# Performance work log

Measured on AMD Instinct MI355X. Metric: run time of the kernel, lower is better.

The kernel has to match this reference:

```python
import jax, jax.numpy as jnp
import numpy as np

B, D1, DJ, S, OUT = 8, 1024, 512, 2048, 2048
IN = D1 + 2 * DJ  # linear input_dim = 2048


def setup_inputs() -> dict:
    key = jax.random.key(0)
    k1, k2, k3, kw, kb = jax.random.split(key, 5)
    return {
        "input1": jax.random.normal(k1, (B, D1, S), dtype=jnp.float32),
        "input2_a": jax.random.normal(k2, (B, DJ, S), dtype=jnp.float32),
        "input2_b": jax.random.normal(k3, (B, DJ, S), dtype=jnp.float32),
        "W": jax.random.normal(kw, (OUT, IN), dtype=jnp.float32) * (1.0 / np.sqrt(IN)),
        "b": jax.random.normal(kb, (OUT,), dtype=jnp.float32) * 0.01,
    }


def reference(input1, input2_a, input2_b, W, b):
    # Original loops over seq_len, per-step concat along feature dim then linear.
    # Fused: concat along feature axis once, transpose to [B, S, F], one GEMM.
    x = jnp.concatenate([input1, input2_a, input2_b], axis=1)  # [B, IN, S]
    x = jnp.transpose(x, (0, 2, 1))                            # [B, S, IN]
    out = jnp.einsum('bsf,of->bso', x, W) + b                  # [B, S, OUT]
    return out
```

## Files before the change

### kernel.cpp

```cpp
#include <hip/hip_runtime.h>
#include <hip/hip_bf16.h>

#define B_   8
#define D1_  1024
#define DJ_  512
#define S_   2048
#define OUT_ 2048
#define IN_  2048
#define M_TOT (B_ * S_)

typedef __attribute__((ext_vector_type(8))) short          bf16x8;
typedef __attribute__((ext_vector_type(8))) unsigned short ushort8;
typedef __attribute__((ext_vector_type(4))) float          f32x4;

typedef __attribute__((address_space(3))) unsigned int as3_uint;
typedef __attribute__((address_space(1))) unsigned int as1_uint;

__device__ __forceinline__ unsigned short f2bf(float f) {
    union { float f; unsigned u; } v; v.f = f;
    unsigned r = v.u + 0x7FFF + ((v.u >> 16) & 1);
    return (unsigned short)(r >> 16);
}

__device__ __forceinline__ void gload_lds16(const void* g, const void* l) {
    __builtin_amdgcn_global_load_lds(
        (const as1_uint*)(unsigned long long)g,
        (as3_uint*)(unsigned int)(unsigned long long)l,
        16, 0, 0);
}

__global__ __launch_bounds__(256) void prep_kernel(
        const float* __restrict__ in1, const float* __restrict__ in2a,
        const float* __restrict__ in2b, const float* __restrict__ W,
        unsigned short* __restrict__ Xt, unsigned short* __restrict__ Wb) {
    int bid = blockIdx.x;
    if (bid >= 8192) {
        size_t i = (size_t)(bid - 8192) * 256 + threadIdx.x;
        const float4* p = reinterpret_cast<const float4*>(W) + i * 2;
        float4 a = p[0], c = p[1];
        ushort8 h;
        h[0] = f2bf(a.x); h[1] = f2bf(a.y); h[2] = f2bf(a.z); h[3] = f2bf(a.w);
        h[4] = f2bf(c.x); h[5] = f2bf(c.y); h[6] = f2bf(c.z); h[7] = f2bf(c.w);
        *(reinterpret_cast<ushort8*>(Wb) + i) = h;
        return;
    }
    __shared__ float tile[64][65];
    int st = bid & 31;
    int ft = (bid >> 5) & 31;
    int b  = bid >> 10;
    int f0 = ft << 6, s0 = st << 6;

    const float* src; int frel;
    if (f0 < D1_)             { src = in1  + (size_t)b * D1_ * S_; frel = f0; }
    else if (f0 < D1_ + DJ_)  { src = in2a + (size_t)b * DJ_ * S_; frel = f0 - D1_; }
    else                      { src = in2b + (size_t)b * DJ_ * S_; frel = f0 - (D1_ + DJ_); }

    int t = threadIdx.x;
    int tr = t >> 4, tc = t & 15;
    #pragma unroll
    for (int i = 0; i < 4; ++i) {
        int fi = tr + i * 16;
        const float4 v = *reinterpret_cast<const float4*>(
            &src[(size_t)(frel + fi) * S_ + s0 + tc * 4]);
        tile[fi][tc * 4 + 0] = v.x; tile[fi][tc * 4 + 1] = v.y;
        tile[fi][tc * 4 + 2] = v.z; tile[fi][tc * 4 + 3] = v.w;
    }
    __syncthreads();
    int si0 = t >> 3, fx = t & 7;
    #pragma unroll
    for (int i = 0; i < 2; ++i) {
        int si = si0 + i * 32;
        ushort8 h;
        #pragma unroll
        for (int j = 0; j < 8; ++j) h[j] = f2bf(tile[fx * 8 + j][si]);
        *reinterpret_cast<ushort8*>(
            &Xt[(size_t)(b * S_ + s0 + si) * IN_ + f0 + fx * 8]) = h;
    }
}


__global__ __launch_bounds__(512, 2) void gemm256_kernel(
        const unsigned short* __restrict__ A,
        const unsigned short* __restrict__ Bm,
        const float* __restrict__ bias,
        float* __restrict__ C) {
    __shared__ unsigned short As_[32768];
    __shared__ unsigned short Bs_[32768];

    int bid = blockIdx.x;
    int swz = (bid & 7) * 64 + (bid >> 3);
    int m0 = (swz >> 3) * 256;
    int n0 = (swz & 7) * 256;

    int t = threadIdx.x;
    int lane = t & 63, wave = t >> 6;
    int wm = wave >> 2;
    int wn = wave & 3;
    int fr = lane & 15;
    int fkslot = lane >> 4;

    int sr  = t >> 3;
    int sc  = t & 7;
    int swc = sc ^ (sr & 7);

    int sl0 = ((fkslot)     ^ (fr & 7)) * 8;
    int sl1 = ((4 + fkslot) ^ (fr & 7)) * 8;
    int arow = wm * 64 + fr;
    int brow = wn * 32 + fr;

#define STAGE_A(bb, h, kt) do { \
    const unsigned short* _g0 = A + (size_t)(m0 + (h)*64 + sr) * IN_ + (kt) + swc*8; \
    const unsigned short* _g1 = A + (size_t)(m0 + 128 + (h)*64 + sr) * IN_ + (kt) + swc*8; \
    unsigned short* _l = As_ + ((bb)*2 + (h))*8192 + sr*64 + sc*8; \
    gload_lds16(_g0, _l); \
    gload_lds16(_g1, _l + 4096); \
} while (0)

#define STAGE_B(bb, h, kt) do { \
    const unsigned short* _g0 = Bm + (size_t)(n0 + (sr>>5)*64 + (h)*32 + (sr&31)) * IN_ + (kt) + swc*8; \
    const unsigned short* _g1 = Bm + (size_t)(n0 + 128 + (sr>>5)*64 + (h)*32 + (sr&31)) * IN_ + (kt) + swc*8; \
    unsigned short* _l = Bs_ + ((bb)*2 + (h))*8192 + sr*64 + sc*8; \
    gload_lds16(_g0, _l); \
    gload_lds16(_g1, _l + 4096); \
} while (0)

#define READ_A(bb, qm) do { \
    const unsigned short* _Ab = As_ + ((bb)*2 + (qm))*8192; \
    _Pragma("unroll") \
    for (int i = 0; i < 4; ++i) { \
        int rr = (arow + i*16) * 64; \
        a_[i][0] = *reinterpret_cast<const bf16x8*>(_Ab + rr + sl0); \
        a_[i][1] = *reinterpret_cast<const bf16x8*>(_Ab + rr + sl1); \
    } \
} while (0)

#define READ_B(bb, qn) do { \
    const unsigned short* _Bb = Bs_ + ((bb)*2 + (qn))*8192; \
    _Pragma("unroll") \
    for (int j = 0; j < 2; ++j) { \
        int rr = (brow + j*16) * 64; \
        b_[j][0] = *reinterpret_cast<const bf16x8*>(_Bb + rr + sl0); \
        b_[j][1] = *reinterpret_cast<const bf16x8*>(_Bb + rr + sl1); \
    } \
} while (0)

#define MFMA4(qm, qn) \
    _Pragma("unroll") \
    for (int i = 0; i < 4; ++i) { \
        _Pragma("unroll") \
        for (int j = 0; j < 2; ++j) { \
            acc[(qm)*4+i][(qn)*2+j] = __builtin_amdgcn_mfma_f32_16x16x32_bf16( \
                a_[i][0], b_[j][0], acc[(qm)*4+i][(qn)*2+j], 0, 0, 0); \
            acc[(qm)*4+i][(qn)*2+j] = __builtin_amdgcn_mfma_f32_16x16x32_bf16( \
                a_[i][1], b_[j][1], acc[(qm)*4+i][(qn)*2+j], 0, 0, 0); \
        } \
    }

#define LGKM0 do { \
    asm volatile("s_waitcnt lgkmcnt(0)" ::: "memory"); \
    __builtin_amdgcn_sched_barrier(0); \
} while (0)

#define VMW asm volatile("s_waitcnt vmcnt(4)" ::: "memory")

#define SP_EVEN(bb, S1, S2, VM_STMT) do { \
    READ_B(bb, 0); \
    READ_A(bb, 0); \
    S1; S2; \
    LGKM0; \
    __builtin_amdgcn_s_setprio(1); \
    MFMA4(0, 0) \
    __builtin_amdgcn_s_setprio(0); \
    READ_B(bb, 1); \
    LGKM0; \
    __builtin_amdgcn_s_setprio(1); \
    MFMA4(0, 1) \
    __builtin_amdgcn_s_setprio(0); \
    VM_STMT; \
    __builtin_amdgcn_s_barrier(); \
} while (0)

#define SP_ODD(bb, S1, S2, VM_STMT) do { \
    READ_A(bb, 1); \
    S1; S2; \
    LGKM0; \
    __builtin_amdgcn_s_setprio(1); \
    MFMA4(1, 1) \
    __builtin_amdgcn_s_setprio(0); \
    READ_B(bb, 0); \
    LGKM0; \
    __builtin_amdgcn_s_setprio(1); \
    MFMA4(1, 0) \
    __builtin_amdgcn_s_setprio(0); \
    VM_STMT; \
    __builtin_amdgcn_s_barrier(); \
} while (0)

    f32x4 acc[8][4] = {};
    bf16x8 a_[4][2], b_[2][2];

    STAGE_A(0, 0, 0);  STAGE_A(0, 1, 0);
    STAGE_B(0, 0, 0);  STAGE_B(0, 1, 0);
    STAGE_A(1, 0, 64); STAGE_B(1, 1, 64);
    asm volatile("s_waitcnt vmcnt(4)" ::: "memory");
    __builtin_amdgcn_s_barrier();

    for (int it = 0; it < IN_ / 128; ++it) {
        int k1 = it * 128 + 64;
        int k2 = (it * 128 + 128) & (IN_ - 1);
        int k3 = (it * 128 + 192) & (IN_ - 1);
        SP_EVEN(0, STAGE_A(1, 1, k1), STAGE_B(1, 0, k1), );
        SP_ODD (0, STAGE_A(0, 0, k2), STAGE_B(0, 1, k2), VMW);
        SP_EVEN(1, STAGE_A(0, 1, k2), STAGE_B(0, 0, k2), );
        SP_ODD (1, STAGE_A(1, 0, k3), STAGE_B(1, 1, k3), VMW);
    }

    float bv[4];
    #pragma unroll
    for (int n_ = 0; n_ < 4; ++n_) bv[n_] = bias[n0 + wn * 64 + n_ * 16 + fr];
    int crow0 = m0 + wm * 128 + (lane >> 4) * 4;
    int ccol0 = n0 + wn * 64 + fr;
    #pragma unroll
    for (int mi = 0; mi < 8; ++mi) {
        #pragma unroll
        for (int r_ = 0; r_ < 4; ++r_) {
            float* cp = C + (size_t)(crow0 + mi * 16 + r_) * OUT_ + ccol0;
            #pragma unroll
            for (int n_ = 0; n_ < 4; ++n_) cp[n_ * 16] = acc[mi][n_][r_] + bv[n_];
        }
    }
#undef STAGE_A
#undef STAGE_B
#undef READ_A
#undef READ_B
#undef MFMA4
#undef LGKM0
#undef VMW
#undef SP_EVEN
#undef SP_ODD
}

__global__ __launch_bounds__(256) void naive_kernel(
        const float* __restrict__ in1, const float* __restrict__ in2a,
        const float* __restrict__ in2b, const float* __restrict__ W,
        const float* __restrict__ bias, float* __restrict__ out) {
    size_t id = (size_t)blockIdx.x * 256 + threadIdx.x;
    int s = (int)(id & (S_ - 1));
    size_t bo = id >> 11;
    int o = (int)(bo & (OUT_ - 1));
    int b = (int)(bo >> 11);
    const float* w = W + (size_t)o * IN_;
    float acc = bias[o];
    const float* x1 = in1 + (size_t)b * D1_ * S_ + s;
    for (int f = 0; f < D1_; ++f) acc += x1[(size_t)f * S_] * w[f];
    const float* x2 = in2a + (size_t)b * DJ_ * S_ + s;
    for (int f = 0; f < DJ_; ++f) acc += x2[(size_t)f * S_] * w[D1_ + f];
    const float* x3 = in2b + (size_t)b * DJ_ * S_ + s;
    for (int f = 0; f < DJ_; ++f) acc += x3[(size_t)f * S_] * w[D1_ + DJ_ + f];
    out[((size_t)b * S_ + s) * OUT_ + o] = acc;
}

extern "C" void kernel_launch(void* const* d_in, const int* in_sizes, int n_in,
                              void* d_out, int out_size, void* d_ws, size_t ws_size,
                              hipStream_t stream) {
    const float* in1  = (const float*)d_in[0];
    const float* in2a = (const float*)d_in[1];
    const float* in2b = (const float*)d_in[2];
    const float* W    = (const float*)d_in[3];
    const float* bias = (const float*)d_in[4];
    float* out = (float*)d_out;

    const size_t xt_bytes = (size_t)M_TOT * IN_ * 2;
    const size_t wb_bytes = (size_t)OUT_ * IN_ * 2;

    if (ws_size < xt_bytes + wb_bytes) {
        naive_kernel<<<(B_ * (size_t)OUT_ * S_) / 256, 256, 0, stream>>>(
            in1, in2a, in2b, W, bias, out);
        return;
    }

    unsigned short* Xt = (unsigned short*)d_ws;
    unsigned short* Wb = (unsigned short*)((char*)d_ws + xt_bytes);

    prep_kernel<<<8192 + (OUT_ * IN_) / (256 * 8), 256, 0, stream>>>(
        in1, in2a, in2b, W, Xt, Wb);
    gemm256_kernel<<<(M_TOT / 256) * (OUT_ / 256), 512, 0, stream>>>(Xt, Wb, bias, out);
}
```

Measured before the change: 162.7 us.

## Fuse activation transpose and bf16 conversion into the GEMM A-tile loader

Removes the separate prep pass that transposed and converted the fp32 activations into a bf16 workspace. The GEMM now loads fp32 activations directly from the three input tensors with per-lane strided register loads, converts them to bf16, and writes them swizzled into LDS. Only W is still converted in a small separate kernel. This avoids writing and re-reading a 64 MB bf16 intermediate. In exchange, the GEMM fetches fp32 A tiles (twice the bytes), re-reads them once per N tile, and adds VALU conversion and LDS-store work inside the pipelined main loop.

Result: slower. 201.4 us (+23.8%).

```diff
diff --git a/kernel.cpp b/kernel.cpp
--- a/kernel.cpp
+++ b/kernel.cpp
@@ -29,58 +29,21 @@
         16, 0, 0);
 }
 
-__global__ __launch_bounds__(256) void prep_kernel(
+__global__ __launch_bounds__(256) void convert_w_kernel(
+        const float* __restrict__ W, unsigned short* __restrict__ Wb) {
+    size_t i = (size_t)blockIdx.x * 256 + threadIdx.x;
+    const float4* p = reinterpret_cast<const float4*>(W) + i * 2;
+    float4 a = p[0], c = p[1];
+    ushort8 h;
+    h[0] = f2bf(a.x); h[1] = f2bf(a.y); h[2] = f2bf(a.z); h[3] = f2bf(a.w);
+    h[4] = f2bf(c.x); h[5] = f2bf(c.y); h[6] = f2bf(c.z); h[7] = f2bf(c.w);
+    *(reinterpret_cast<ushort8*>(Wb) + i) = h;
+}
+
+
+__global__ __launch_bounds__(512, 2) void gemm256_kernel(
         const float* __restrict__ in1, const float* __restrict__ in2a,
-        const float* __restrict__ in2b, const float* __restrict__ W,
-        unsigned short* __restrict__ Xt, unsigned short* __restrict__ Wb) {
-    int bid = blockIdx.x;
-    if (bid >= 8192) {
-        size_t i = (size_t)(bid - 8192) * 256 + threadIdx.x;
-        const float4* p = reinterpret_cast<const float4*>(W) + i * 2;
-        float4 a = p[0], c = p[1];
-        ushort8 h;
-        h[0] = f2bf(a.x); h[1] = f2bf(a.y); h[2] = f2bf(a.z); h[3] = f2bf(a.w);
-        h[4] = f2bf(c.x); h[5] = f2bf(c.y); h[6] = f2bf(c.z); h[7] = f2bf(c.w);
-        *(reinterpret_cast<ushort8*>(Wb) + i) = h;
-        return;
-    }
-    __shared__ float tile[64][65];
-    int st = bid & 31;
-    int ft = (bid >> 5) & 31;
-    int b  = bid >> 10;
-    int f0 = ft << 6, s0 = st << 6;
-
-    const float* src; int frel;
-    if (f0 < D1_)             { src = in1  + (size_t)b * D1_ * S_; frel = f0; }
-    else if (f0 < D1_ + DJ_)  { src = in2a + (size_t)b * DJ_ * S_; frel = f0 - D1_; }
-    else                      { src = in2b + (size_t)b * DJ_ * S_; frel = f0 - (D1_ + DJ_); }
-
-    int t = threadIdx.x;
-    int tr = t >> 4, tc = t & 15;
-    #pragma unroll
-    for (int i = 0; i < 4; ++i) {
-        int fi = tr + i * 16;
-        const float4 v = *reinterpret_cast<const float4*>(
-            &src[(size_t)(frel + fi) * S_ + s0 + tc * 4]);
-        tile[fi][tc * 4 + 0] = v.x; tile[fi][tc * 4 + 1] = v.y;
-        tile[fi][tc * 4 + 2] = v.z; tile[fi][tc * 4 + 3] = v.w;
-    }
-    __syncthreads();
-    int si0 = t >> 3, fx = t & 7;
-    #pragma unroll
-    for (int i = 0; i < 2; ++i) {
-        int si = si0 + i * 32;
-        ushort8 h;
-        #pragma unroll
-        for (int j = 0; j < 8; ++j) h[j] = f2bf(tile[fx * 8 + j][si]);
-        *reinterpret_cast<ushort8*>(
-            &Xt[(size_t)(b * S_ + s0 + si) * IN_ + f0 + fx * 8]) = h;
-    }
-}
-
-
-__global__ __launch_bounds__(512, 2) void gemm256_kernel(
-        const unsigned short* __restrict__ A,
+        const float* __restrict__ in2b,
         const unsigned short* __restrict__ Bm,
         const float* __restrict__ bias,
         float* __restrict__ C) {
@@ -108,12 +71,34 @@
     int arow = wm * 64 + fr;
     int brow = wn * 32 + fr;
 
-#define STAGE_A(bb, h, kt) do { \
-    const unsigned short* _g0 = A + (size_t)(m0 + (h)*64 + sr) * IN_ + (kt) + swc*8; \
-    const unsigned short* _g1 = A + (size_t)(m0 + 128 + (h)*64 + sr) * IN_ + (kt) + swc*8; \
-    unsigned short* _l = As_ + ((bb)*2 + (h))*8192 + sr*64 + sc*8; \
-    gload_lds16(_g0, _l); \
-    gload_lds16(_g1, _l + 4096); \
+    int b_idx = m0 >> 11;
+    int s0g   = m0 & 2047;
+    const size_t sb1 = (size_t)b_idx * D1_ * S_;
+    const size_t sb2 = (size_t)b_idx * DJ_ * S_;
+
+#define ABASE(ktn_) ((ktn_) < 1024 \
+        ? in1 + sb1 + (size_t)(ktn_) * S_ + s0g \
+        : ((ktn_) < 1536 \
+            ? in2a + sb2 + (size_t)((ktn_) - 1024) * S_ + s0g \
+            : in2b + sb2 + (size_t)((ktn_) - 1536) * S_ + s0g))
+
+#define AU_LOAD(REG, u) do { \
+    int _idx = wave * 4 + (u); int _fg = _idx & 7; \
+    int _so = ((_idx >> 3) << 6) + lane; \
+    _Pragma("unroll") \
+    for (int _k = 0; _k < 8; ++_k) \
+        REG[_k] = ab[(size_t)(_fg * 8 + _k) * S_ + _so]; \
+} while (0)
+
+#define AU_CW(REG, u, bbn) do { \
+    int _idx = wave * 4 + (u); int _fg = _idx & 7; \
+    int _g = ((_idx >> 3) << 6) + lane; \
+    int _qm = (_g >> 6) & 1; int _lr = ((_g >> 7) << 6) | (_g & 63); \
+    ushort8 _h; \
+    _Pragma("unroll") \
+    for (int _k = 0; _k < 8; ++_k) _h[_k] = f2bf(REG[_k]); \
+    *reinterpret_cast<ushort8*>( \
+        As_ + ((bbn)*2 + _qm)*8192 + _lr*64 + (_fg ^ (_lr & 7))*8) = _h; \
 } while (0)
 
 #define STAGE_B(bb, h, kt) do { \
@@ -161,58 +146,71 @@
     __builtin_amdgcn_sched_barrier(0); \
 } while (0)
 
-#define VMW asm volatile("s_waitcnt vmcnt(4)" ::: "memory")
-
-#define SP_EVEN(bb, S1, S2, VM_STMT) do { \
+#define VMN(n) do { \
+    asm volatile("s_waitcnt vmcnt(" #n ")" ::: "memory"); \
+    __builtin_amdgcn_sched_barrier(0); \
+} while (0)
+
+#define SP(bb) do { \
+    AU_LOAD(avA, 0); \
+    AU_LOAD(avB, 1); \
+    STAGE_B(bb^1, 0, ktn); \
+    STAGE_B(bb^1, 1, ktn); \
+    READ_B(bb, 0); READ_A(bb, 0); \
+    LGKM0; \
+    __builtin_amdgcn_s_setprio(1); \
+    MFMA4(0, 0) \
+    __builtin_amdgcn_s_setprio(0); \
+    VMN(12); \
+    AU_CW(avA, 0, bb^1); \
+    AU_LOAD(avA, 2); \
+    READ_B(bb, 1); \
+    LGKM0; \
+    __builtin_amdgcn_s_setprio(1); \
+    MFMA4(0, 1) \
+    __builtin_amdgcn_s_setprio(0); \
+    VMN(12); \
+    AU_CW(avB, 1, bb^1); \
+    AU_LOAD(avB, 3); \
+    READ_A(bb, 1); \
+    LGKM0; \
+    __builtin_amdgcn_s_setprio(1); \
+    MFMA4(1, 1) \
+    __builtin_amdgcn_s_setprio(0); \
+    VMN(8); \
+    AU_CW(avA, 2, bb^1); \
     READ_B(bb, 0); \
-    READ_A(bb, 0); \
-    S1; S2; \
-    LGKM0; \
-    __builtin_amdgcn_s_setprio(1); \
-    MFMA4(0, 0) \
-    __builtin_amdgcn_s_setprio(0); \
-    READ_B(bb, 1); \
-    LGKM0; \
-    __builtin_amdgcn_s_setprio(1); \
-    MFMA4(0, 1) \
-    __builtin_amdgcn_s_setprio(0); \
-    VM_STMT; \
-    __builtin_amdgcn_s_barrier(); \
-} while (0)
-
-#define SP_ODD(bb, S1, S2, VM_STMT) do { \
-    READ_A(bb, 1); \
-    S1; S2; \
-    LGKM0; \
-    __builtin_amdgcn_s_setprio(1); \
-    MFMA4(1, 1) \
-    __builtin_amdgcn_s_setprio(0); \
-    READ_B(bb, 0); \
     LGKM0; \
     __builtin_amdgcn_s_setprio(1); \
     MFMA4(1, 0) \
     __builtin_amdgcn_s_setprio(0); \
-    VM_STMT; \
+    VMN(0); \
+    AU_CW(avB, 3, bb^1); \
+    asm volatile("s_waitcnt lgkmcnt(0)" ::: "memory"); \
     __builtin_amdgcn_s_barrier(); \
 } while (0)
 
     f32x4 acc[8][4] = {};
     bf16x8 a_[4][2], b_[2][2];
-
-    STAGE_A(0, 0, 0);  STAGE_A(0, 1, 0);
-    STAGE_B(0, 0, 0);  STAGE_B(0, 1, 0);
-    STAGE_A(1, 0, 64); STAGE_B(1, 1, 64);
-    asm volatile("s_waitcnt vmcnt(4)" ::: "memory");
-    __builtin_amdgcn_s_barrier();
+    float avA[8], avB[8];
+
+    {
+        const float* ab = ABASE(0);
+        AU_LOAD(avA, 0); AU_LOAD(avB, 1);
+        STAGE_B(0, 0, 0); STAGE_B(0, 1, 0);
+        VMN(12); AU_CW(avA, 0, 0); AU_LOAD(avA, 2);
+        VMN(12); AU_CW(avB, 1, 0); AU_LOAD(avB, 3);
+        VMN(8);  AU_CW(avA, 2, 0);
+        VMN(0);  AU_CW(avB, 3, 0);
+        asm volatile("s_waitcnt lgkmcnt(0)" ::: "memory");
+        __builtin_amdgcn_s_barrier();
+    }
 
     for (int it = 0; it < IN_ / 128; ++it) {
-        int k1 = it * 128 + 64;
-        int k2 = (it * 128 + 128) & (IN_ - 1);
-        int k3 = (it * 128 + 192) & (IN_ - 1);
-        SP_EVEN(0, STAGE_A(1, 1, k1), STAGE_B(1, 0, k1), );
-        SP_ODD (0, STAGE_A(0, 0, k2), STAGE_B(0, 1, k2), VMW);
-        SP_EVEN(1, STAGE_A(0, 1, k2), STAGE_B(0, 0, k2), );
-        SP_ODD (1, STAGE_A(1, 0, k3), STAGE_B(1, 1, k3), VMW);
+        int kt1 = it * 128 + 64;
+        int kt2 = (it * 128 + 128) & (IN_ - 1);
+        { const float* ab = ABASE(kt1); int ktn = kt1; SP(0); }
+        { const float* ab = ABASE(kt2); int ktn = kt2; SP(1); }
     }
 
     float bv[4];
@@ -229,15 +227,16 @@
             for (int n_ = 0; n_ < 4; ++n_) cp[n_ * 16] = acc[mi][n_][r_] + bv[n_];
         }
     }
-#undef STAGE_A
+#undef ABASE
+#undef AU_LOAD
+#undef AU_CW
 #undef STAGE_B
 #undef READ_A
 #undef READ_B
 #undef MFMA4
 #undef LGKM0
-#undef VMW
-#undef SP_EVEN
-#undef SP_ODD
+#undef VMN
+#undef SP
 }
 
 __global__ __launch_bounds__(256) void naive_kernel(
@@ -270,19 +269,17 @@
     const float* bias = (const float*)d_in[4];
     float* out = (float*)d_out;
 
-    const size_t xt_bytes = (size_t)M_TOT * IN_ * 2;
     const size_t wb_bytes = (size_t)OUT_ * IN_ * 2;
 
-    if (ws_size < xt_bytes + wb_bytes) {
+    if (ws_size < wb_bytes) {
         naive_kernel<<<(B_ * (size_t)OUT_ * S_) / 256, 256, 0, stream>>>(
             in1, in2a, in2b, W, bias, out);
         return;
     }
 
-    unsigned short* Xt = (unsigned short*)d_ws;
-    unsigned short* Wb = (unsigned short*)((char*)d_ws + xt_bytes);
-
-    prep_kernel<<<8192 + (OUT_ * IN_) / (256 * 8), 256, 0, stream>>>(
-        in1, in2a, in2b, W, Xt, Wb);
-    gemm256_kernel<<<(M_TOT / 256) * (OUT_ / 256), 512, 0, stream>>>(Xt, Wb, bias, out);
-}
+    unsigned short* Wb = (unsigned short*)d_ws;
+
+    convert_w_kernel<<<(OUT_ * IN_) / (256 * 8), 256, 0, stream>>>(W, Wb);
+    gemm256_kernel<<<(M_TOT / 256) * (OUT_ / 256), 512, 0, stream>>>(
+        in1, in2a, in2b, Wb, bias, out);
+}
```

## Load B operand directly from global into registers, dropping B LDS staging

Applied to the files above, without the earlier changes.

Removes the shared-memory buffer for the weight operand. Each wave now loads its B fragments straight from global memory into double-buffered registers, while A stays staged through LDS. The main loop is restructured into a single two-stage pipeline, and the block swizzle is replaced with a plain row-major tile mapping. This halves LDS use and cuts LDS read traffic, which could allow higher occupancy. In exchange it adds many uncoalesced global loads, with each wave's B rows duplicated across waves, plus register pressure and possibly worse L2 locality.

Result: slower. 215.9 us (+32.7%).

```diff
diff --git a/kernel.cpp b/kernel.cpp
--- a/kernel.cpp
+++ b/kernel.cpp
@@ -85,12 +85,11 @@
         const float* __restrict__ bias,
         float* __restrict__ C) {
     __shared__ unsigned short As_[32768];
-    __shared__ unsigned short Bs_[32768];
 
     int bid = blockIdx.x;
-    int swz = (bid & 7) * 64 + (bid >> 3);
-    int m0 = (swz >> 3) * 256;
-    int n0 = (swz & 7) * 256;
+    int ntile = bid & 7;
+    int mtile = bid >> 3;
+    int m0 = mtile * 256, n0 = ntile * 256;
 
     int t = threadIdx.x;
     int lane = t & 63, wave = t >> 6;
@@ -106,20 +105,11 @@
     int sl0 = ((fkslot)     ^ (fr & 7)) * 8;
     int sl1 = ((4 + fkslot) ^ (fr & 7)) * 8;
     int arow = wm * 64 + fr;
-    int brow = wn * 32 + fr;
 
 #define STAGE_A(bb, h, kt) do { \
     const unsigned short* _g0 = A + (size_t)(m0 + (h)*64 + sr) * IN_ + (kt) + swc*8; \
     const unsigned short* _g1 = A + (size_t)(m0 + 128 + (h)*64 + sr) * IN_ + (kt) + swc*8; \
     unsigned short* _l = As_ + ((bb)*2 + (h))*8192 + sr*64 + sc*8; \
-    gload_lds16(_g0, _l); \
-    gload_lds16(_g1, _l + 4096); \
-} while (0)
-
-#define STAGE_B(bb, h, kt) do { \
-    const unsigned short* _g0 = Bm + (size_t)(n0 + (sr>>5)*64 + (h)*32 + (sr&31)) * IN_ + (kt) + swc*8; \
-    const unsigned short* _g1 = Bm + (size_t)(n0 + 128 + (sr>>5)*64 + (h)*32 + (sr&31)) * IN_ + (kt) + swc*8; \
-    unsigned short* _l = Bs_ + ((bb)*2 + (h))*8192 + sr*64 + sc*8; \
     gload_lds16(_g0, _l); \
     gload_lds16(_g1, _l + 4096); \
 } while (0)
@@ -134,25 +124,27 @@
     } \
 } while (0)
 
-#define READ_B(bb, qn) do { \
-    const unsigned short* _Bb = Bs_ + ((bb)*2 + (qn))*8192; \
+#define LOADB_Q(DST, qn, ktn) do { \
     _Pragma("unroll") \
-    for (int j = 0; j < 2; ++j) { \
-        int rr = (brow + j*16) * 64; \
-        b_[j][0] = *reinterpret_cast<const bf16x8*>(_Bb + rr + sl0); \
-        b_[j][1] = *reinterpret_cast<const bf16x8*>(_Bb + rr + sl1); \
+    for (int _j = 0; _j < 2; ++_j) { \
+        _Pragma("unroll") \
+        for (int _kk = 0; _kk < 2; ++_kk) { \
+            DST[_j][_kk] = *reinterpret_cast<const bf16x8*>( \
+                Bm + (size_t)(n0 + wn*64 + (qn)*32 + _j*16 + fr) * IN_ \
+                   + (ktn) + _kk*32 + fkslot*8); \
+        } \
     } \
 } while (0)
 
-#define MFMA4(qm, qn) \
+#define MFMA4(qm, qn, BS) \
     _Pragma("unroll") \
     for (int i = 0; i < 4; ++i) { \
         _Pragma("unroll") \
         for (int j = 0; j < 2; ++j) { \
             acc[(qm)*4+i][(qn)*2+j] = __builtin_amdgcn_mfma_f32_16x16x32_bf16( \
-                a_[i][0], b_[j][0], acc[(qm)*4+i][(qn)*2+j], 0, 0, 0); \
+                a_[i][0], BS[j][0], acc[(qm)*4+i][(qn)*2+j], 0, 0, 0); \
             acc[(qm)*4+i][(qn)*2+j] = __builtin_amdgcn_mfma_f32_16x16x32_bf16( \
-                a_[i][1], b_[j][1], acc[(qm)*4+i][(qn)*2+j], 0, 0, 0); \
+                a_[i][1], BS[j][1], acc[(qm)*4+i][(qn)*2+j], 0, 0, 0); \
         } \
     }
 
@@ -161,58 +153,49 @@
     __builtin_amdgcn_sched_barrier(0); \
 } while (0)
 
-#define VMW asm volatile("s_waitcnt vmcnt(4)" ::: "memory")
-
-#define SP_EVEN(bb, S1, S2, VM_STMT) do { \
-    READ_B(bb, 0); \
+#define VMN(n) do { \
+    asm volatile("s_waitcnt vmcnt(" #n ")" ::: "memory"); \
+    __builtin_amdgcn_sched_barrier(0); \
+} while (0)
+
+#define SP(bb, BC0, BC1, BN0, BN1, ktn) do { \
+    STAGE_A((bb)^1, 0, ktn); \
+    STAGE_A((bb)^1, 1, ktn); \
+    LOADB_Q(BN0, 0, ktn); \
     READ_A(bb, 0); \
-    S1; S2; \
+    VMN(8); \
     LGKM0; \
     __builtin_amdgcn_s_setprio(1); \
-    MFMA4(0, 0) \
+    MFMA4(0, 0, BC0) \
+    MFMA4(0, 1, BC1) \
     __builtin_amdgcn_s_setprio(0); \
-    READ_B(bb, 1); \
+    READ_A(bb, 1); \
+    LOADB_Q(BN1, 1, ktn); \
     LGKM0; \
     __builtin_amdgcn_s_setprio(1); \
-    MFMA4(0, 1) \
+    MFMA4(1, 1, BC1) \
+    MFMA4(1, 0, BC0) \
     __builtin_amdgcn_s_setprio(0); \
-    VM_STMT; \
+    VMN(8); \
     __builtin_amdgcn_s_barrier(); \
 } while (0)
 
-#define SP_ODD(bb, S1, S2, VM_STMT) do { \
-    READ_A(bb, 1); \
-    S1; S2; \
-    LGKM0; \
-    __builtin_amdgcn_s_setprio(1); \
-    MFMA4(1, 1) \
-    __builtin_amdgcn_s_setprio(0); \
-    READ_B(bb, 0); \
-    LGKM0; \
-    __builtin_amdgcn_s_setprio(1); \
-    MFMA4(1, 0) \
-    __builtin_amdgcn_s_setprio(0); \
-    VM_STMT; \
-    __builtin_amdgcn_s_barrier(); \
-} while (0)
-
     f32x4 acc[8][4] = {};
-    bf16x8 a_[4][2], b_[2][2];
-
-    STAGE_A(0, 0, 0);  STAGE_A(0, 1, 0);
-    STAGE_B(0, 0, 0);  STAGE_B(0, 1, 0);
-    STAGE_A(1, 0, 64); STAGE_B(1, 1, 64);
-    asm volatile("s_waitcnt vmcnt(4)" ::: "memory");
+    bf16x8 a_[4][2];
+    bf16x8 bq0A[2][2], bq1A[2][2], bq0B[2][2], bq1B[2][2];
+
+    STAGE_A(0, 0, 0);
+    STAGE_A(0, 1, 0);
+    LOADB_Q(bq0A, 0, 0);
+    LOADB_Q(bq1A, 1, 0);
+    VMN(0);
     __builtin_amdgcn_s_barrier();
 
     for (int it = 0; it < IN_ / 128; ++it) {
         int k1 = it * 128 + 64;
         int k2 = (it * 128 + 128) & (IN_ - 1);
-        int k3 = (it * 128 + 192) & (IN_ - 1);
-        SP_EVEN(0, STAGE_A(1, 1, k1), STAGE_B(1, 0, k1), );
-        SP_ODD (0, STAGE_A(0, 0, k2), STAGE_B(0, 1, k2), VMW);
-        SP_EVEN(1, STAGE_A(0, 1, k2), STAGE_B(0, 0, k2), );
-        SP_ODD (1, STAGE_A(1, 0, k3), STAGE_B(1, 1, k3), VMW);
+        SP(0, bq0A, bq1A, bq0B, bq1B, k1);
+        SP(1, bq0B, bq1B, bq0A, bq1A, k2);
     }
 
     float bv[4];
@@ -230,14 +213,12 @@
         }
     }
 #undef STAGE_A
-#undef STAGE_B
 #undef READ_A
-#undef READ_B
+#undef LOADB_Q
 #undef MFMA4
 #undef LGKM0
-#undef VMW
-#undef SP_EVEN
-#undef SP_ODD
+#undef VMN
+#undef SP
 }
 
 __global__ __launch_bounds__(256) void naive_kernel(
```

## Replace split half-tile pipeline with simple full-tile double buffering

Applied to the files above, without the earlier changes.

Replaces the four-phase schedule, which staged half-tiles of A and B interleaved across even/odd sub-phases with partial vmcnt waits, with a two-phase double-buffered loop. Each phase issues all four global-to-LDS loads for the next K tile up front, then reads B and A from LDS and runs all MFMA quadrants before a full vmcnt(0) wait and barrier. B fragments are kept in two register sets so B is read from LDS once per phase instead of twice. This simplifies the schedule and cuts LDS reads, but waits on all outstanding loads each phase, so memory latency may be less hidden and barrier stalls may grow.

Result: no change. 165.4 us (+1.6%).

```diff
diff --git a/kernel.cpp b/kernel.cpp
--- a/kernel.cpp
+++ b/kernel.cpp
@@ -134,25 +134,25 @@
     } \
 } while (0)
 
-#define READ_B(bb, qn) do { \
+#define READ_B(bb, qn, DST) do { \
     const unsigned short* _Bb = Bs_ + ((bb)*2 + (qn))*8192; \
     _Pragma("unroll") \
     for (int j = 0; j < 2; ++j) { \
         int rr = (brow + j*16) * 64; \
-        b_[j][0] = *reinterpret_cast<const bf16x8*>(_Bb + rr + sl0); \
-        b_[j][1] = *reinterpret_cast<const bf16x8*>(_Bb + rr + sl1); \
+        DST[j][0] = *reinterpret_cast<const bf16x8*>(_Bb + rr + sl0); \
+        DST[j][1] = *reinterpret_cast<const bf16x8*>(_Bb + rr + sl1); \
     } \
 } while (0)
 
-#define MFMA4(qm, qn) \
+#define MFMA4(qm, qn, BS) \
     _Pragma("unroll") \
     for (int i = 0; i < 4; ++i) { \
         _Pragma("unroll") \
         for (int j = 0; j < 2; ++j) { \
             acc[(qm)*4+i][(qn)*2+j] = __builtin_amdgcn_mfma_f32_16x16x32_bf16( \
-                a_[i][0], b_[j][0], acc[(qm)*4+i][(qn)*2+j], 0, 0, 0); \
+                a_[i][0], BS[j][0], acc[(qm)*4+i][(qn)*2+j], 0, 0, 0); \
             acc[(qm)*4+i][(qn)*2+j] = __builtin_amdgcn_mfma_f32_16x16x32_bf16( \
-                a_[i][1], b_[j][1], acc[(qm)*4+i][(qn)*2+j], 0, 0, 0); \
+                a_[i][1], BS[j][1], acc[(qm)*4+i][(qn)*2+j], 0, 0, 0); \
         } \
     }
 
@@ -161,58 +161,45 @@
     __builtin_amdgcn_sched_barrier(0); \
 } while (0)
 
-#define VMW asm volatile("s_waitcnt vmcnt(4)" ::: "memory")
-
-#define SP_EVEN(bb, S1, S2, VM_STMT) do { \
-    READ_B(bb, 0); \
-    READ_A(bb, 0); \
-    S1; S2; \
+#define SP(p, ktn) do { \
+    STAGE_A((p)^1, 0, ktn); \
+    STAGE_A((p)^1, 1, ktn); \
+    STAGE_B((p)^1, 0, ktn); \
+    STAGE_B((p)^1, 1, ktn); \
+    READ_B(p, 0, b0_); \
+    READ_A(p, 0); \
     LGKM0; \
     __builtin_amdgcn_s_setprio(1); \
-    MFMA4(0, 0) \
+    MFMA4(0, 0, b0_) \
     __builtin_amdgcn_s_setprio(0); \
-    READ_B(bb, 1); \
+    READ_B(p, 1, b1_); \
     LGKM0; \
     __builtin_amdgcn_s_setprio(1); \
-    MFMA4(0, 1) \
+    MFMA4(0, 1, b1_) \
     __builtin_amdgcn_s_setprio(0); \
-    VM_STMT; \
-    __builtin_amdgcn_s_barrier(); \
-} while (0)
-
-#define SP_ODD(bb, S1, S2, VM_STMT) do { \
-    READ_A(bb, 1); \
-    S1; S2; \
+    READ_A(p, 1); \
     LGKM0; \
     __builtin_amdgcn_s_setprio(1); \
-    MFMA4(1, 1) \
+    MFMA4(1, 1, b1_) \
+    MFMA4(1, 0, b0_) \
     __builtin_amdgcn_s_setprio(0); \
-    READ_B(bb, 0); \
-    LGKM0; \
-    __builtin_amdgcn_s_setprio(1); \
-    MFMA4(1, 0) \
-    __builtin_amdgcn_s_setprio(0); \
-    VM_STMT; \
+    asm volatile("s_waitcnt vmcnt(0)" ::: "memory"); \
     __builtin_amdgcn_s_barrier(); \
 } while (0)
 
     f32x4 acc[8][4] = {};
-    bf16x8 a_[4][2], b_[2][2];
-
-    STAGE_A(0, 0, 0);  STAGE_A(0, 1, 0);
-    STAGE_B(0, 0, 0);  STAGE_B(0, 1, 0);
-    STAGE_A(1, 0, 64); STAGE_B(1, 1, 64);
-    asm volatile("s_waitcnt vmcnt(4)" ::: "memory");
+    bf16x8 a_[4][2], b0_[2][2], b1_[2][2];
+
+    STAGE_A(0, 0, 0); STAGE_A(0, 1, 0);
+    STAGE_B(0, 0, 0); STAGE_B(0, 1, 0);
+    asm volatile("s_waitcnt vmcnt(0)" ::: "memory");
     __builtin_amdgcn_s_barrier();
 
     for (int it = 0; it < IN_ / 128; ++it) {
         int k1 = it * 128 + 64;
         int k2 = (it * 128 + 128) & (IN_ - 1);
-        int k3 = (it * 128 + 192) & (IN_ - 1);
-        SP_EVEN(0, STAGE_A(1, 1, k1), STAGE_B(1, 0, k1), );
-        SP_ODD (0, STAGE_A(0, 0, k2), STAGE_B(0, 1, k2), VMW);
-        SP_EVEN(1, STAGE_A(0, 1, k2), STAGE_B(0, 0, k2), );
-        SP_ODD (1, STAGE_A(1, 0, k3), STAGE_B(1, 1, k3), VMW);
+        SP(0, k1);
+        SP(1, k2);
     }
 
     float bv[4];
@@ -235,9 +222,7 @@
 #undef READ_B
 #undef MFMA4
 #undef LGKM0
-#undef VMW
-#undef SP_EVEN
-#undef SP_ODD
+#undef SP
 }
 
 __global__ __launch_bounds__(256) void naive_kernel(
```
